# Optimization experiments

Measured on AMD Instinct MI355X. Metric: run time of the kernel, lower is better.

The kernel has to match this reference:

```python
import jax, jax.numpy as jnp
import numpy as np

C = 512
NUM_GROUPS = 4
EPS = 1e-6


def _conv1x1(W, b, t):
    # 1x1x1 Conv3d == per-position linear over channels
    return jnp.einsum('oc,bcfhw->bofhw', W, t) + b[None, :, None, None, None]


def setup_inputs() -> dict:
    key = jax.random.key(0)
    ks = jax.random.split(key, 11)
    c = C
    x = jax.random.normal(ks[0], (12, c, 48, 48), dtype=jnp.float32)
    p = lambda k: jax.random.normal(k, (c, c), dtype=jnp.float32) * 0.02
    return {
        'x': x,
        'norm_scale': jnp.ones((c,), jnp.float32),
        'norm_bias': jnp.zeros((c,), jnp.float32),
        'q_w': p(ks[1]), 'q_b': jnp.zeros((c,), jnp.float32),
        'k_w': p(ks[2]), 'k_b': jnp.zeros((c,), jnp.float32),
        'v_w': p(ks[3]), 'v_b': jnp.zeros((c,), jnp.float32),
        'proj_w': p(ks[4]), 'proj_b': jnp.zeros((c,), jnp.float32),
    }


def reference(x, norm_scale, norm_bias, q_w, q_b, k_w, k_b, v_w, v_b, proj_w, proj_b):
    b3, c, h, w = x.shape
    b = b3 // 3
    # chunk batch into 3 frames, stack at frame dim -> (b, c, 3, h, w)
    h_ = jnp.stack(jnp.split(x, 3, axis=0), axis=2)
    # GroupNorm(num_groups=4) over (C/G, F, H, W) per group
    g = NUM_GROUPS
    xg = h_.reshape(b, g, c // g, 3, h, w)
    mean = jnp.mean(xg, axis=(2, 3, 4, 5), keepdims=True)
    var = jnp.var(xg, axis=(2, 3, 4, 5), keepdims=True)
    xn = ((xg - mean) * jax.lax.rsqrt(var + EPS)).reshape(b, c, 3, h, w)
    hn = xn * norm_scale[None, :, None, None, None] + norm_bias[None, :, None, None, None]
    q = _conv1x1(q_w, q_b, hn)[:, :, 1:2]          # middle frame only: (b,c,1,h,w)
    skip = q[:, :, 0]                               # (b,c,h,w)
    k = _conv1x1(k_w, k_b, hn)                      # (b,c,3,h,w)
    v = _conv1x1(v_w, v_b, hn)
    n = h * w
    qf = q.reshape(b, c, n)                         # (b,c,n)
    kf = k.reshape(b, c, 3 * n)                     # (b,c,3n)
    vf = v.reshape(b, c, 3 * n)
    scores = jnp.einsum('bcn,bcm->bnm', qf, kf) * (float(c) ** -0.5)
    attn = jax.nn.softmax(scores, axis=2)           # (b,n,3n)
    out = jnp.einsum('bcm,bnm->bcn', vf, attn).reshape(b, c, 1, h, w)
    out = _conv1x1(proj_w, proj_b, out)[:, :, 0]
    return skip + out
```

## Files before the change

kernel.cpp:

```cpp
#include <hip/hip_runtime.h>

typedef unsigned short u16;
typedef unsigned long long u64;
typedef __attribute__((ext_vector_type(8))) short short8;
typedef __attribute__((ext_vector_type(4))) float f32x4;

__device__ __forceinline__ float bf2f(u16 h) {
    union { unsigned int u; float f; } v; v.u = ((unsigned int)h) << 16; return v.f;
}
__device__ __forceinline__ u16 f2bf(float f) {
    union { float f; unsigned int u; } v; v.f = f;
    unsigned int r = v.u + 0x7fffu + ((v.u >> 16) & 1u);
    return (u16)(r >> 16);
}

__device__ __forceinline__ void gload16(const u16* g, u16* l) {
    __builtin_amdgcn_global_load_lds(
        (const __attribute__((address_space(1))) void*)g,
        (__attribute__((address_space(3))) void*)l,
        16, 0, 0);
}

template<int N> __device__ __forceinline__ void waitvm() {
    static_assert(N >= 0 && N <= 12, "enumerate more");
    if constexpr (N == 0)  asm volatile("s_waitcnt vmcnt(0)"  ::: "memory");
    else if constexpr (N == 1)  asm volatile("s_waitcnt vmcnt(1)"  ::: "memory");
    else if constexpr (N == 2)  asm volatile("s_waitcnt vmcnt(2)"  ::: "memory");
    else if constexpr (N == 3)  asm volatile("s_waitcnt vmcnt(3)"  ::: "memory");
    else if constexpr (N == 4)  asm volatile("s_waitcnt vmcnt(4)"  ::: "memory");
    else if constexpr (N == 5)  asm volatile("s_waitcnt vmcnt(5)"  ::: "memory");
    else if constexpr (N == 6)  asm volatile("s_waitcnt vmcnt(6)"  ::: "memory");
    else if constexpr (N == 7)  asm volatile("s_waitcnt vmcnt(7)"  ::: "memory");
    else if constexpr (N == 8)  asm volatile("s_waitcnt vmcnt(8)"  ::: "memory");
    else if constexpr (N == 9)  asm volatile("s_waitcnt vmcnt(9)"  ::: "memory");
    else if constexpr (N == 10) asm volatile("s_waitcnt vmcnt(10)" ::: "memory");
    else if constexpr (N == 11) asm volatile("s_waitcnt vmcnt(11)" ::: "memory");
    else                        asm volatile("s_waitcnt vmcnt(12)" ::: "memory");
}

__device__ __forceinline__ float waveSum(float v) {
#pragma unroll
    for (int o = 32; o > 0; o >>= 1) v += __shfl_down(v, o);
    return v;
}
__device__ __forceinline__ float waveMax(float v) {
#pragma unroll
    for (int o = 32; o > 0; o >>= 1) v = fmaxf(v, __shfl_down(v, o));
    return v;
}
__device__ __forceinline__ int waveSumI(int v) {
#pragma unroll
    for (int o = 32; o > 0; o >>= 1) v += __shfl_down(v, o);
    return v;
}

__global__ __launch_bounds__(256) void detect_k(const u16* __restrict__ x, int* __restrict__ flag) {
    __shared__ int cnt[4];
    int c = 0;
    for (int i = threadIdx.x; i < 8192; i += 256) {
        u16 e = x[i * 2];
        int ex = (e >> 7) & 0xFF;
        c += (ex == 0 || (ex >= 100 && ex <= 150)) ? 1 : 0;
    }
    c = waveSumI(c);
    if ((threadIdx.x & 63) == 0) cnt[threadIdx.x >> 6] = c;
    __syncthreads();
    if (threadIdx.x == 0)
        flag[0] = ((cnt[0] + cnt[1] + cnt[2] + cnt[3]) > 4915) ? 1 : 0;
}

__global__ __launch_bounds__(256) void conv_k(const void* __restrict__ src, u16* __restrict__ dst,
                                              int n8, const int* __restrict__ flag) {
    int i = blockIdx.x * 256 + threadIdx.x;
    if (i >= n8) return;
    if (flag[0]) {
        ((int4*)dst)[i] = ((const int4*)src)[i];
    } else {
        const float* f = (const float*)src + (size_t)i * 8;
        union { int4 v4; u16 o[8]; } tv;
#pragma unroll
        for (int j = 0; j < 8; j++) tv.o[j] = f2bf(f[j]);
        ((int4*)dst)[i] = tv.v4;
    }
}

__global__ __launch_bounds__(256) void conv_w4(const void* s0, const void* s1, const void* s2, const void* s3,
                                               u16* __restrict__ dst, const int* __restrict__ flag) {
    int i = blockIdx.x * 256 + threadIdx.x;
    int w = blockIdx.y;
    const void* s = w == 0 ? s0 : w == 1 ? s1 : w == 2 ? s2 : s3;
    u16* d = dst + (size_t)w * 262144;
    if (flag[0]) {
        ((int4*)d)[i] = ((const int4*)s)[i];
    } else {
        const float* f = (const float*)s + (size_t)i * 8;
        union { int4 v4; u16 o[8]; } tv;
#pragma unroll
        for (int j = 0; j < 8; j++) tv.o[j] = f2bf(f[j]);
        ((int4*)d)[i] = tv.v4;
    }
}

__global__ __launch_bounds__(256) void conv_v6(const void* s0, const void* s1, const void* s2,
                                               const void* s3, const void* s4, const void* s5,
                                               u16* __restrict__ dst, const int* __restrict__ flag) {
    for (int i = threadIdx.x; i < 384; i += 256) {
        int seg = i >> 6, off = i & 63;
        const void* s = seg == 0 ? s0 : seg == 1 ? s1 : seg == 2 ? s2 : seg == 3 ? s3 : seg == 4 ? s4 : s5;
        u16* d = dst + (size_t)seg * 512;
        if (flag[0]) {
            ((int4*)d)[off] = ((const int4*)s)[off];
        } else {
            const float* f = (const float*)s + (size_t)off * 8;
            union { int4 v4; u16 o[8]; } tv;
#pragma unroll
            for (int j = 0; j < 8; j++) tv.o[j] = f2bf(f[j]);
            ((int4*)d)[off] = tv.v4;
        }
    }
}

__global__ __launch_bounds__(256) void gn_stats(const u16* __restrict__ x, float* __restrict__ stat) {
    __shared__ float red[8];
    const int gg = blockIdx.y, chunk = blockIdx.x;
    const int b = gg >> 2, g = gg & 3;
    float s = 0.f, s2 = 0.f;
    for (int pp = 0; pp < 12; pp++) {
        int p = chunk * 12 + pp;
        int t = p >> 7, cc = p & 127;
        const u16* rowp = x + (size_t)((t * 4 + b) * 512 + g * 128 + cc) * 2304;
        for (int vi = threadIdx.x; vi < 288; vi += 256) {
            union { int4 v4; u16 u[8]; } tv;
            tv.v4 = *(const int4*)(rowp + vi * 8);
#pragma unroll
            for (int j = 0; j < 8; j++) { float f = bf2f(tv.u[j]); s += f; s2 += f * f; }
        }
    }
    s = waveSum(s); s2 = waveSum(s2);
    int wid = threadIdx.x >> 6;
    if ((threadIdx.x & 63) == 0) { red[wid] = s; red[wid + 4] = s2; }
    __syncthreads();
    if (threadIdx.x == 0) {
        atomicAdd(&stat[gg], red[0] + red[1] + red[2] + red[3]);
        atomicAdd(&stat[16 + gg], red[4] + red[5] + red[6] + red[7]);
    }
}

__global__ void gn_ab(const float* __restrict__ stat, const u16* __restrict__ scale,
                      const u16* __restrict__ bias, float2* __restrict__ ab) {
    int idx = blockIdx.x * 256 + threadIdx.x;
    int b = idx >> 9, c = idx & 511, g = c >> 7, gg = b * 4 + g;
    const float invN = 1.f / 884736.f;
    float mean = stat[gg] * invN;
    float var  = stat[16 + gg] * invN - mean * mean;
    float rstd = rsqrtf(var + 1e-6f);
    float a = rstd * bf2f(scale[c]);
    ab[idx] = make_float2(a, bf2f(bias[c]) - mean * a);
}

__global__ __launch_bounds__(256) void normT_k(const u16* __restrict__ xb,
                                               const float2* __restrict__ ab,
                                               u16* __restrict__ xnT) {
    __shared__ u16 t[64][72];
    const int zz = blockIdx.z;
    const int b = zz & 3, tt = zz >> 2;
    const u16* s = xb + (size_t)zz * 512 * 2304;
    u16* d = xnT + (size_t)b * (512L * 6912) + (size_t)tt * 2304 * 512;
    const int c0 = blockIdx.x * 64;
    const int r0 = blockIdx.y * 64;
    const int tid = threadIdx.x;
#pragma unroll
    for (int p = 0; p < 4; p++) {
        int r = p * 16 + (tid >> 4);
        int c4 = (tid & 15) * 4;
        float2 sab = ab[b * 512 + r0 + r];
        union { u64 u; u16 e[4]; } tv;
        tv.u = *(const u64*)(s + (size_t)(r0 + r) * 2304 + c0 + c4);
#pragma unroll
        for (int j = 0; j < 4; j++) t[r][c4 + j] = f2bf(bf2f(tv.e[j]) * sab.x + sab.y);
    }
    __syncthreads();
#pragma unroll
    for (int p = 0; p < 2; p++) {
        int n = p * 32 + (tid >> 3);
        int c8 = (tid & 7) * 8;
        union { int4 v4; u16 o[8]; } tv;
#pragma unroll
        for (int j = 0; j < 8; j++) tv.o[j] = t[c8 + j][n];
        *(int4*)(d + (size_t)(c0 + n) * 512 + r0 + c8) = tv.v4;
    }
}

template<int WR, int WC, int TI, int TJ, int AMODE, int BMODE, int EPI, int F32OUT, int SPLITK, int SWZ>
__global__ __launch_bounds__(256)
void gemm_k(const u16* __restrict__ A, const u16* __restrict__ B, void* __restrict__ Cv,
            const u16* __restrict__ bias, const u16* __restrict__ skip,
            const float2* __restrict__ ab,
            int lda, int ldb, int ldc,
            int K, float alpha, int m_off, int b0,
            long aZS, long bZS, long cZS, long sZS) {
    constexpr int BM = WR * TI * 16;
    constexpr int BN = WC * TJ * 16;
    constexpr bool PIPE = (AMODE == 0 && BMODE == 1);
    constexpr int NBUF = PIPE ? ((BM + BN <= 192) ? 4 : 3) : 2;
    constexpr int LDA_S = (AMODE == 0) ? 32 : 44;
    constexpr int LDB_S = (BMODE == 1) ? 32 : 44;
    __shared__ alignas(16) u16 As[NBUF][BM][LDA_S];
    __shared__ alignas(16) u16 Bs[NBUF][BN][LDB_S];

    int bxi = blockIdx.x, byi = blockIdx.y, bzi = blockIdx.z;
    if (SWZ) {
        int gx = gridDim.x, gy = gridDim.y;
        long NN = (long)gx * gy * gridDim.z;
        long L = bxi + (long)gx * (byi + (long)gy * bzi);
        long q = NN >> 3, r = NN & 7;
        long xc = L & 7, m = L >> 3;
        long nl = (xc < r ? xc * (q + 1) : r * (q + 1) + (xc - r) * q) + m;
        bxi = (int)(nl % gx);
        long t2 = nl / gx;
        byi = (int)(t2 % gy);
        bzi = (int)(t2 / gy);
    }

    const int tid = threadIdx.x;
    const int z = bzi;
    const int i0b = byi * BM;
    const int j0b = bxi * BN;
    const int kstart = SPLITK ? z * K : 0;

    const u16* Ap = A + (size_t)z * aZS;
    const u16* Bp;
    const float2* abp = nullptr;
    int yx0 = 0;
    if (BMODE == 2) {
        int b = b0 + (SPLITK ? 0 : z);
        int m_tile = j0b + m_off;
        int t = m_tile / 2304;
        yx0 = m_tile - t * 2304;
        Bp = B + (size_t)((t * 4 + b) * 512) * 2304;
        abp = ab + b * 512;
    } else {
        Bp = B + (size_t)z * bZS;
    }
    const u16* Sp = (EPI & 10) ? (skip + (size_t)z * sZS) : nullptr;
    float* Cf = (float*)Cv + (size_t)z * (F32OUT ? cZS : 0);
    u16*   Ch = (u16*)Cv   + (size_t)z * (F32OUT ? 0 : cZS);

    const int wave = tid >> 6;
    const int lane = tid & 63;
    const int wr = wave / WC;
    const int wc = wave % WC;
    const int lrow = lane & 15;
    const int quad = lane >> 4;
    const int sws = ((quad ^ ((lrow >> 1) & 3)) << 3);

    auto stage = [&](int bsel, int k0) {
        if (AMODE == 0) {
            constexpr int NV = (BM * 32 / 8) / 256;
#pragma unroll
            for (int v = 0; v < NV; v++) {
                int vid = tid + v * 256;
                int i = vid >> 2;
                int ks = (((vid & 3) ^ ((vid >> 3) & 3)) * 8);
                gload16(Ap + (size_t)(i0b + i) * lda + (k0 + ks), &As[bsel][i][(vid & 3) * 8]);
            }
        } else {
            constexpr int NV = (BM * 32 / 8) / 256;
            constexpr int IG = BM / 8;
#pragma unroll
            for (int v = 0; v < NV; v++) {
                int vid = tid + v * 256;
                int k = vid / IG, ib = (vid % IG) * 8;
                union { int4 v4; u16 s[8]; } tv;
                tv.v4 = *(const int4*)(Ap + (size_t)(k0 + k) * lda + (i0b + ib));
#pragma unroll
                for (int j = 0; j < 8; j++) As[bsel][ib + j][k] = tv.s[j];
            }
        }
        if (BMODE == 1) {
            constexpr int NV = (BN * 32 / 8) / 256;
#pragma unroll
            for (int v = 0; v < NV; v++) {
                int vid = tid + v * 256;
                int j = vid >> 2;
                int ks = (((vid & 3) ^ ((vid >> 3) & 3)) * 8);
                gload16(Bp + (size_t)(j0b + j) * ldb + (k0 + ks), &Bs[bsel][j][(vid & 3) * 8]);
            }
        } else {
            constexpr int NV = (BN * 32 / 8) / 256;
            constexpr int JG = BN / 8;
#pragma unroll
            for (int v = 0; v < NV; v++) {
                int vid = tid + v * 256;
                int k = vid / JG, jb = (vid % JG) * 8;
                if (BMODE == 0) {
                    union { int4 v4; u16 s[8]; } tv;
                    tv.v4 = *(const int4*)(Bp + (size_t)(k0 + k) * ldb + (j0b + jb));
#pragma unroll
                    for (int j = 0; j < 8; j++) Bs[bsel][jb + j][k] = tv.s[j];
                } else {
                    union { int4 v4; u16 s[8]; } tv;
                    tv.v4 = *(const int4*)(Bp + (size_t)(k0 + k) * 2304 + (yx0 + jb));
                    float2 amb = abp[k0 + k];
#pragma unroll
                    for (int j = 0; j < 8; j++)
                        Bs[bsel][jb + j][k] = f2bf(bf2f(tv.s[j]) * amb.x + amb.y);
                }
            }
        }
    };

    f32x4 acc[TI][TJ] = {};

    auto compute = [&](int bsel) {
        union FragU { short8 v; u64 u[2]; int4 v4; };
        FragU fa[TI], fb[TJ];
#pragma unroll
        for (int ri = 0; ri < TI; ri++) {
            int r = wr * TI * 16 + ri * 16 + lrow;
            if constexpr (LDA_S == 32) {
                fa[ri].v4 = *(const int4*)(&As[bsel][r][sws]);
            } else {
                fa[ri].u[0] = *(const u64*)(&As[bsel][r][quad * 8]);
                fa[ri].u[1] = *(const u64*)(&As[bsel][r][quad * 8 + 4]);
            }
        }
#pragma unroll
        for (int cj = 0; cj < TJ; cj++) {
            int cc2 = wc * TJ * 16 + cj * 16 + lrow;
            if constexpr (LDB_S == 32) {
                fb[cj].v4 = *(const int4*)(&Bs[bsel][cc2][sws]);
            } else {
                fb[cj].u[0] = *(const u64*)(&Bs[bsel][cc2][quad * 8]);
                fb[cj].u[1] = *(const u64*)(&Bs[bsel][cc2][quad * 8 + 4]);
            }
        }
        if constexpr (PIPE) __builtin_amdgcn_s_setprio(1);
#pragma unroll
        for (int ri = 0; ri < TI; ri++)
#pragma unroll
            for (int cj = 0; cj < TJ; cj++)
                acc[ri][cj] = __builtin_amdgcn_mfma_f32_16x16x32_bf16(
                    fa[ri].v, fb[cj].v, acc[ri][cj], 0, 0, 0);
        if constexpr (PIPE) __builtin_amdgcn_s_setprio(0);
    };

    const int kend = kstart + K;

    if constexpr (PIPE) {
        constexpr int LPS = (BM * 32 / 8) / 256 + (BN * 32 / 8) / 256;
        constexpr int D = NBUF - 2;
        const int NT = K / 32;
        for (int t = 0; t < D && t < NT; ++t) stage(t, kstart + t * 32);
        int cur = 0;
        for (int t = 0; t < NT; ++t) {
            if (t + D < NT) {
                int tgt = cur + D; if (tgt >= NBUF) tgt -= NBUF;
                stage(tgt, kstart + (t + D) * 32);
            }
            const int rem = NT - 1 - t;
            if (rem >= D)      waitvm<D * LPS>();
            else if (rem == 1) waitvm<LPS>();
            else               waitvm<0>();
            __builtin_amdgcn_s_barrier();
            __builtin_amdgcn_sched_barrier(0);
            compute(cur);
            cur = (cur + 1 == NBUF) ? 0 : cur + 1;
        }
    } else {
        stage(0, kstart);
        __syncthreads();
        int cur = 0;
        for (int k0 = kstart; k0 < kend; k0 += 32) {
            if (k0 + 32 < kend) stage(cur ^ 1, k0 + 32);
            compute(cur);
            __syncthreads();
            cur ^= 1;
        }
    }

#pragma unroll
    for (int ri = 0; ri < TI; ri++) {
#pragma unroll
        for (int reg = 0; reg < 4; reg++) {
            int gi = i0b + wr * TI * 16 + ri * 16 + quad * 4 + reg;
            float bv = (EPI & 1) ? bf2f(bias[gi]) : 0.f;
#pragma unroll
            for (int cj = 0; cj < TJ; cj++) {
                int gj = j0b + wc * TJ * 16 + cj * 16 + lrow;
                float v = acc[ri][cj][reg] * alpha + bv;
                if (EPI & 4) v += bf2f(bias[gj]);
                if (EPI & 2) v += bf2f(Sp[(size_t)gi * ldc + gj]);
                if (EPI & 8) v += bf2f(Sp[(size_t)gj * 512 + gi]);
                if (F32OUT) Cf[(size_t)gi * ldc + gj] = v;
                else        Ch[(size_t)gi * ldc + gj] = f2bf(v);
            }
        }
    }
}

__global__ __launch_bounds__(256) void softmax_k(u16* __restrict__ sb, long zs) {
    __shared__ float row[6912];
    __shared__ float red[8];
    u16* p = sb + (size_t)blockIdx.y * zs + (size_t)blockIdx.x * 6912;
    const int tid = threadIdx.x;
    float mx = -3.0e38f;
    for (int vi = tid; vi < 864; vi += 256) {
        union { int4 v4; u16 u[8]; } tv;
        tv.v4 = *(const int4*)(p + vi * 8);
#pragma unroll
        for (int j = 0; j < 8; j++) { float f = bf2f(tv.u[j]); row[vi * 8 + j] = f; mx = fmaxf(mx, f); }
    }
    mx = waveMax(mx);
    if ((tid & 63) == 0) red[tid >> 6] = mx;
    __syncthreads();
    mx = fmaxf(fmaxf(red[0], red[1]), fmaxf(red[2], red[3]));
    __syncthreads();
    float sum = 0.f;
    for (int i = tid; i < 6912; i += 256) {
        float e = __expf(row[i] - mx);
        row[i] = e; sum += e;
    }
    sum = waveSum(sum);
    if ((tid & 63) == 0) red[4 + (tid >> 6)] = sum;
    __syncthreads();
    float inv = 1.f / (red[4] + red[5] + red[6] + red[7]);
    for (int vi = tid; vi < 864; vi += 256) {
        union { int4 v4; u16 u[8]; } tv;
#pragma unroll
        for (int j = 0; j < 8; j++) tv.u[j] = f2bf(row[vi * 8 + j] * inv);
        *(int4*)(p + vi * 8) = tv.v4;
    }
}

extern "C" void kernel_launch(void* const* d_in, const int* in_sizes, int n_in,
                              void* d_out, int out_size, void* d_ws, size_t ws_size,
                              hipStream_t stream) {
    float* out = (float*)d_out;

    const long QS = (long)512 * 2304;
    const long KS = (long)512 * 6912;
    const long SS = (long)2304 * 6912;
    const long PS = (long)512 * 2304;
    const float rs = 0.044194173824159216f;

    const size_t FIXED = 256 + 256 + 2048 * sizeof(float2)
                       + (size_t)14155776 * 2 + (size_t)4 * 262144 * 2 + 8192
                       + (size_t)14155776 * 2;
    const size_t PERNB = (size_t)(QS + KS + KS + QS + SS) * 2;
    int nb = 0;
    if      (ws_size >= FIXED + 4 * PERNB) nb = 4;
    else if (ws_size >= FIXED + 2 * PERNB) nb = 2;
    else if (ws_size >= FIXED + 1 * PERNB) nb = 1;

    char* w = (char*)d_ws;
    int*    flag = (int*)w;     w += 256;
    float*  stat = (float*)w;   w += 256;
    float2* ab   = (float2*)w;  w += 2048 * sizeof(float2);
    u16* xb = (u16*)w;  w += (size_t)14155776 * 2;
    u16* wgt = (u16*)w; w += (size_t)4 * 262144 * 2;
    u16* vecb = (u16*)w; w += 8192;

    detect_k<<<1, 256, 0, stream>>>((const u16*)d_in[0], flag);
    conv_k<<<6912, 256, 0, stream>>>(d_in[0], xb, 1769472, flag);
    conv_w4<<<dim3(128, 4), 256, 0, stream>>>(d_in[3], d_in[5], d_in[7], d_in[9], wgt, flag);
    conv_v6<<<1, 256, 0, stream>>>(d_in[1], d_in[2], d_in[4], d_in[6], d_in[8], d_in[10], vecb, flag);
    hipMemsetAsync(stat, 0, 32 * sizeof(float), stream);
    gn_stats<<<dim3(32, 16), 256, 0, stream>>>(xb, stat);
    gn_ab<<<8, 256, 0, stream>>>(stat, vecb, vecb + 512, ab);

    const u16* qw = wgt;
    const u16* kw = wgt + 262144;
    const u16* vw = wgt + 2 * 262144;
    const u16* pw = wgt + 3 * 262144;
    const u16* qb2 = vecb + 1024, *kb2 = vecb + 1536, *vb2 = vecb + 2048, *pb2 = vecb + 2560;

    if (nb == 0) {
        u16* qbuf = (u16*)w;  w += QS * 2;
        u16* kbuf = (u16*)w;  w += KS * 2;
        u16* vbuf = (u16*)w;  w += KS * 2;
        u16* obuf = (u16*)w;  w += QS * 2;
        u16* sbuf = (u16*)w;
        for (int b = 0; b < 4; b++) {
            gemm_k<2,2,4,4,0,2,1,0,0,0><<<dim3(54,4,1),256,0,stream>>>(
                kw, xb, kbuf, kb2, nullptr, ab, 512,0,6912, 512,1.f,0,b, 0,0,0,0);
            gemm_k<2,2,4,4,0,2,1,0,0,0><<<dim3(54,4,1),256,0,stream>>>(
                vw, xb, vbuf, vb2, nullptr, ab, 512,0,6912, 512,1.f,0,b, 0,0,0,0);
            gemm_k<2,2,4,4,0,2,1,0,0,0><<<dim3(18,4,1),256,0,stream>>>(
                qw, xb, qbuf, qb2, nullptr, ab, 512,0,2304, 512,1.f,2304,b, 0,0,0,0);
            gemm_k<2,2,4,4,1,0,0,0,0,0><<<dim3(54,18,1),256,0,stream>>>(
                qbuf, kbuf, sbuf, nullptr,nullptr,nullptr, 2304,6912,6912, 512,rs,0,b, 0,0,0,0);
            softmax_k<<<dim3(2304,1),256,0,stream>>>(sbuf, 0);
            gemm_k<1,4,4,1,0,1,0,0,0,0><<<dim3(36,8,1),256,0,stream>>>(
                vbuf, sbuf, obuf, nullptr,nullptr,nullptr, 6912,6912,2304, 6912,1.f,0,b, 0,0,0,0);
            gemm_k<2,2,4,2,0,0,3,1,0,0><<<dim3(36,4,1),256,0,stream>>>(
                pw, obuf, out + (size_t)b * PS, pb2, qbuf, nullptr,
                512,2304,2304, 512,1.f,0,b, 0,0,0,0);
        }
        return;
    }

    u16* xnT = (u16*)w; w += (size_t)14155776 * 2;
    u16* qT  = (u16*)w; w += (size_t)nb * QS * 2;
    u16* kT  = (u16*)w; w += (size_t)nb * KS * 2;
    u16* vbuf= (u16*)w; w += (size_t)nb * KS * 2;
    u16* obT = (u16*)w; w += (size_t)nb * QS * 2;
    u16* sbuf= (u16*)w; w += (size_t)nb * SS * 2;

    normT_k<<<dim3(36, 8, 12), 256, 0, stream>>>(xb, ab, xnT);

    for (int g = 0; g < 4; g += nb) {
        gemm_k<2,2,4,4,0,1,4,0,0,1><<<dim3(4,54,nb),256,0,stream>>>(
            xnT + (size_t)g * KS, kw, kT, kb2, nullptr, nullptr,
            512,512,512, 512,1.f,0,g, KS,0,KS,0);
        gemm_k<2,2,4,4,0,1,4,0,0,1><<<dim3(4,18,nb),256,0,stream>>>(
            xnT + (size_t)g * KS + (size_t)2304 * 512, qw, qT, qb2, nullptr, nullptr,
            512,512,512, 512,1.f,0,g, KS,0,QS,0);
        gemm_k<2,2,4,4,0,1,1,0,0,1><<<dim3(54,4,nb),256,0,stream>>>(
            vw, xnT + (size_t)g * KS, vbuf, vb2, nullptr, nullptr,
            512,512,6912, 512,1.f,0,g, 0,KS,KS,0);
        gemm_k<2,2,4,4,0,1,0,0,0,1><<<dim3(54,18,nb),256,0,stream>>>(
            qT, kT, sbuf, nullptr,nullptr,nullptr, 512,512,6912, 512,rs,0,g, QS,KS,SS,0);
        softmax_k<<<dim3(2304,nb),256,0,stream>>>(sbuf, SS);
        gemm_k<2,2,2,4,0,1,0,0,0,1><<<dim3(4,36,nb),256,0,stream>>>(
            sbuf, vbuf, obT, nullptr,nullptr,nullptr, 6912,6912,512, 6912,1.f,0,g, SS,KS,QS,0);
        gemm_k<2,2,4,2,0,1,9,1,0,1><<<dim3(36,4,nb),256,0,stream>>>(
            pw, obT, out + (size_t)g * PS, pb2, qT, nullptr,
            512,512,2304, 512,1.f,0,g, 0,QS,PS,QS);
    }
}
```

Baseline: 497.1 us.

## Add AMODE 2 GEMM path loading B fragments directly to registers for PV

```diff
diff --git a/kernel.cpp b/kernel.cpp
--- a/kernel.cpp
+++ b/kernel.cpp
@@ -22,7 +22,7 @@
 }
 
 template<int N> __device__ __forceinline__ void waitvm() {
-    static_assert(N >= 0 && N <= 12, "enumerate more");
+    static_assert(N >= 0 && N <= 16, "enumerate more");
     if constexpr (N == 0)  asm volatile("s_waitcnt vmcnt(0)"  ::: "memory");
     else if constexpr (N == 1)  asm volatile("s_waitcnt vmcnt(1)"  ::: "memory");
     else if constexpr (N == 2)  asm volatile("s_waitcnt vmcnt(2)"  ::: "memory");
@@ -35,7 +35,11 @@
     else if constexpr (N == 9)  asm volatile("s_waitcnt vmcnt(9)"  ::: "memory");
     else if constexpr (N == 10) asm volatile("s_waitcnt vmcnt(10)" ::: "memory");
     else if constexpr (N == 11) asm volatile("s_waitcnt vmcnt(11)" ::: "memory");
-    else                        asm volatile("s_waitcnt vmcnt(12)" ::: "memory");
+    else if constexpr (N == 12) asm volatile("s_waitcnt vmcnt(12)" ::: "memory");
+    else if constexpr (N == 13) asm volatile("s_waitcnt vmcnt(13)" ::: "memory");
+    else if constexpr (N == 14) asm volatile("s_waitcnt vmcnt(14)" ::: "memory");
+    else if constexpr (N == 15) asm volatile("s_waitcnt vmcnt(15)" ::: "memory");
+    else                        asm volatile("s_waitcnt vmcnt(16)" ::: "memory");
 }
 
 __device__ __forceinline__ float waveSum(float v) {
@@ -203,10 +207,13 @@
     constexpr int BN = WC * TJ * 16;
     constexpr bool PIPE = (AMODE == 0 && BMODE == 1);
     constexpr int NBUF = PIPE ? ((BM + BN <= 192) ? 4 : 3) : 2;
-    constexpr int LDA_S = (AMODE == 0) ? 32 : 44;
+    constexpr int NBUFA = (AMODE == 2) ? 6 : NBUF;
+    constexpr int LDA_S = (AMODE != 1) ? 32 : 44;
     constexpr int LDB_S = (BMODE == 1) ? 32 : 44;
-    __shared__ alignas(16) u16 As[NBUF][BM][LDA_S];
-    __shared__ alignas(16) u16 Bs[NBUF][BN][LDB_S];
+    constexpr int BSN  = (AMODE == 2) ? 1 : NBUF;
+    constexpr int BSB  = (AMODE == 2) ? 1 : BN;
+    __shared__ alignas(16) u16 As[NBUFA][BM][LDA_S];
+    __shared__ alignas(16) u16 Bs[BSN][BSB][LDB_S];
 
     int bxi = blockIdx.x, byi = blockIdx.y, bzi = blockIdx.z;
     if (SWZ) {
@@ -264,7 +271,7 @@
                 int ks = (((vid & 3) ^ ((vid >> 3) & 3)) * 8);
                 gload16(Ap + (size_t)(i0b + i) * lda + (k0 + ks), &As[bsel][i][(vid & 3) * 8]);
             }
-        } else {
+        } else if (AMODE == 1) {
             constexpr int NV = (BM * 32 / 8) / 256;
             constexpr int IG = BM / 8;
 #pragma unroll
@@ -277,7 +284,7 @@
                 for (int j = 0; j < 8; j++) As[bsel][ib + j][k] = tv.s[j];
             }
         }
-        if (BMODE == 1) {
+        if (BMODE == 1 && AMODE != 2) {
             constexpr int NV = (BN * 32 / 8) / 256;
 #pragma unroll
             for (int v = 0; v < NV; v++) {
@@ -286,7 +293,7 @@
                 int ks = (((vid & 3) ^ ((vid >> 3) & 3)) * 8);
                 gload16(Bp + (size_t)(j0b + j) * ldb + (k0 + ks), &Bs[bsel][j][(vid & 3) * 8]);
             }
-        } else {
+        } else if (BMODE != 1) {
             constexpr int NV = (BN * 32 / 8) / 256;
             constexpr int JG = BN / 8;
 #pragma unroll
@@ -347,7 +354,65 @@
 
     const int kend = kstart + K;
 
-    if constexpr (PIPE) {
+    if constexpr (AMODE == 2) {
+        const int NT = K / 32;
+        constexpr int NVA = (BM * 32 / 8) / 256;
+        constexpr int W0 = 4 * NVA + TJ;
+        constexpr int W1 = 4 * NVA + 2 * TJ;
+        constexpr int WS = 2 * (NVA + TJ);
+        union FragU3 { short8 v; int4 v4; };
+        FragU3 br0[TJ], br1[TJ], br2[TJ], br3[TJ];
+        const u16* BpJ = Bp + (size_t)(j0b + wc * TJ * 16 + lrow) * ldb + quad * 8;
+        auto stageA = [&](int bsel, int k0) {
+#pragma unroll
+            for (int v = 0; v < NVA; v++) {
+                int vid = tid + v * 256;
+                int i = vid >> 2;
+                int ks = (((vid & 3) ^ ((vid >> 3) & 3)) * 8);
+                gload16(Ap + (size_t)(i0b + i) * lda + (k0 + ks), &As[bsel][i][(vid & 3) * 8]);
+            }
+        };
+#define LOADB3(BR, KO) { _Pragma("unroll") \
+        for (int cj = 0; cj < TJ; cj++) \
+            (BR)[cj].v4 = *(const int4*)(BpJ + (size_t)cj * 16 * ldb + (KO)); }
+#define COMP3(AB, BR) { \
+        FragU3 fa3[TI]; \
+        _Pragma("unroll") for (int ri = 0; ri < TI; ri++) { \
+            int r = wr * TI * 16 + ri * 16 + lrow; \
+            fa3[ri].v4 = *(const int4*)(&As[AB][r][sws]); } \
+        __builtin_amdgcn_s_setprio(1); \
+        _Pragma("unroll") for (int ri = 0; ri < TI; ri++) \
+        _Pragma("unroll") for (int cj = 0; cj < TJ; cj++) \
+            acc[ri][cj] = __builtin_amdgcn_mfma_f32_16x16x32_bf16( \
+                fa3[ri].v, (BR)[cj].v, acc[ri][cj], 0, 0, 0); \
+        __builtin_amdgcn_s_setprio(0); }
+#define STEP3(T, BRU, BRL, WN) { \
+        if ((T) + 4 < NT) stageA(((T) + 4) % 6, kstart + ((T) + 4) * 32); \
+        if ((T) + 2 < NT) LOADB3(BRL, kstart + ((T) + 2) * 32); \
+        if ((T) + 4 < NT) { waitvm<WN>(); } else { waitvm<0>(); } \
+        __builtin_amdgcn_s_barrier(); \
+        __builtin_amdgcn_sched_barrier(0); \
+        COMP3((T) % 6, BRU); }
+        LOADB3(br0, kstart);
+        if (NT > 1) LOADB3(br1, kstart + 32);
+        stageA(0, kstart);
+        if (NT > 1) stageA(1, kstart + 32);
+        if (NT > 2) stageA(2, kstart + 64);
+        if (NT > 3) stageA(3, kstart + 96);
+        STEP3(0, br0, br2, W0);
+        if (NT > 1) STEP3(1, br1, br3, W1);
+        if (NT > 2) STEP3(2, br2, br0, WS);
+        if (NT > 3) STEP3(3, br3, br1, WS);
+        for (int tt = 4; tt + 3 < NT; tt += 4) {
+            STEP3(tt + 0, br0, br2, WS);
+            STEP3(tt + 1, br1, br3, WS);
+            STEP3(tt + 2, br2, br0, WS);
+            STEP3(tt + 3, br3, br1, WS);
+        }
+#undef LOADB3
+#undef COMP3
+#undef STEP3
+    } else if constexpr (PIPE) {
         constexpr int LPS = (BM * 32 / 8) / 256 + (BN * 32 / 8) / 256;
         constexpr int D = NBUF - 2;
         const int NT = K / 32;
@@ -522,7 +587,7 @@
         gemm_k<2,2,4,4,0,1,0,0,0,1><<<dim3(54,18,nb),256,0,stream>>>(
             qT, kT, sbuf, nullptr,nullptr,nullptr, 512,512,6912, 512,rs,0,g, QS,KS,SS,0);
         softmax_k<<<dim3(2304,nb),256,0,stream>>>(sbuf, SS);
-        gemm_k<2,2,2,4,0,1,0,0,0,1><<<dim3(4,36,nb),256,0,stream>>>(
+        gemm_k<2,2,2,4,2,1,0,0,0,1><<<dim3(4,36,nb),256,0,stream>>>(
             sbuf, vbuf, obT, nullptr,nullptr,nullptr, 6912,6912,512, 6912,1.f,0,g, SS,KS,QS,0);
         gemm_k<2,2,4,2,0,1,9,1,0,1><<<dim3(36,4,nb),256,0,stream>>>(
             pw, obT, out + (size_t)g * PS, pb2, qT, nullptr,
```

Result: slower. 701.7 us (+41.2%).
